# Kernel optimization log

Hardware: AMD Instinct MI355X
Metric: run time of the kernel (lower is better)

## Reference

```python
import jax, jax.numpy as jnp
import numpy as np


def setup_inputs() -> dict:
    key = jax.random.key(0)
    k1, k2, k3, k4 = jax.random.split(key, 4)
    B, S, D, R = 32, 512, 1024, 256
    batch = jax.random.normal(k1, (B, S, D), dtype=jnp.float32)
    # params initialized uniform(-0.05, 0.05) in the original
    proj_L = jax.random.uniform(k2, (D, R), minval=-0.05, maxval=0.05, dtype=jnp.float32)
    proj_R = jax.random.uniform(k3, (R, D), minval=-0.05, maxval=0.05, dtype=jnp.float32)
    bias = jax.random.uniform(k4, (1,), minval=-0.05, maxval=0.05, dtype=jnp.float32)
    return {"batch": batch, "proj_L": proj_L, "proj_R": proj_R, "bias": bias}


def reference(batch, proj_L, proj_R, bias):
    # logits[b,i,j] = batch[b,i] @ (L @ R) @ batch[b,j] + bias
    # Computed as (batch @ L) @ (batch @ R^T)^T -- two batched GEMMs,
    # avoiding the O(B*S^2*D) expanded intermediate of the original.
    # Dropout is identity in eval mode.
    left = jnp.einsum('bsd,dr->bsr', batch, proj_L)   # [B,S,R]
    right = jnp.einsum('rd,btd->brt', proj_R, batch)  # [B,R,S]
    logits = jnp.einsum('bsr,brt->bst', left, right) + bias[0]
    return logits
```

## Files before the change

### kernel.cpp

```cpp
#include <hip/hip_runtime.h>
#include <hip/hip_bf16.h>
#include <stdint.h>

typedef __attribute__((ext_vector_type(8))) __bf16 bf16x8;
typedef __attribute__((ext_vector_type(4))) float f32x4;

static constexpr int Bb = 32, Ss = 512, Dd = 1024, Rr = 256;

__device__ __forceinline__ void gload_lds16(const void* g, void* l) {
  __builtin_amdgcn_global_load_lds(
      (const __attribute__((address_space(1))) void*)g,
      (__attribute__((address_space(3))) void*)l, 16, 0, 0);
}

__global__ __launch_bounds__(256) void prep_kernel(
    const float* __restrict__ L, const float* __restrict__ R,
    __bf16* __restrict__ Bt) {
  int i = blockIdx.x * 256 + threadIdx.x;
  int n = i >> 10;
  int d = i & (Dd - 1);
  float v = (n < Rr) ? L[d * Rr + n] : R[(size_t)(n - Rr) * Dd + d];
  Bt[i] = (__bf16)v;
}

__global__ __launch_bounds__(256, 3) void proj_gemm(
    const float* __restrict__ batch,
    const __bf16* __restrict__ Bt,
    __bf16* __restrict__ outL,
    __bf16* __restrict__ outR) {
  const int s = ((blockIdx.x & 7) << 7) + (blockIdx.x >> 3);
  const int mt = s >> 2;
  const int nt = s & 3;
  const int m0 = mt * 64, n0 = nt * 128;

  __shared__ __align__(16) char smem[49152];

  const int t = threadIdx.x;
  const int lane = t & 63;
  const int wave = t >> 6;
  const int wr = wave >> 1, wc = wave & 1;

  f32x4 acc[2][4] = {};
  f32x4 areg[4];

  const int arow = t >> 2, ag = t & 3;
  const int ags = ag ^ (arow & 7);

  auto issueA = [&](int k0) {
    const float* src = batch + (size_t)(m0 + arow) * Dd + k0 + ag * 8;
    areg[0] = *(const f32x4*)src;
    areg[1] = *(const f32x4*)(src + 4);
    areg[2] = *(const f32x4*)(src + 32);
    areg[3] = *(const f32x4*)(src + 36);
  };
  auto writeA = [&](int buf) {
    char* Ab = smem + buf * 8192;
    bf16x8 v0, v1;
    v0[0] = (__bf16)areg[0][0]; v0[1] = (__bf16)areg[0][1];
    v0[2] = (__bf16)areg[0][2]; v0[3] = (__bf16)areg[0][3];
    v0[4] = (__bf16)areg[1][0]; v0[5] = (__bf16)areg[1][1];
    v0[6] = (__bf16)areg[1][2]; v0[7] = (__bf16)areg[1][3];
    v1[0] = (__bf16)areg[2][0]; v1[1] = (__bf16)areg[2][1];
    v1[2] = (__bf16)areg[2][2]; v1[3] = (__bf16)areg[2][3];
    v1[4] = (__bf16)areg[3][0]; v1[5] = (__bf16)areg[3][1];
    v1[6] = (__bf16)areg[3][2]; v1[7] = (__bf16)areg[3][3];
    *(bf16x8*)(Ab + (arow * 8 + ags) * 16) = v0;
    *(bf16x8*)(Ab + (arow * 8 + (ags ^ 4)) * 16) = v1;
  };
  auto stageB = [&](int buf, int k0) {
    char* Bbuf = smem + 16384 + buf * 16384;
#pragma unroll
    for (int p = 0; p < 4; ++p) {
      int e = p * 256 + t;
      int row = e >> 3, g = e & 7;
      int gs = g ^ (row & 7);
      gload_lds16(Bt + (size_t)(n0 + row) * Dd + k0 + gs * 8,
                  Bbuf + e * 16);
    }
  };
  auto compute = [&](int buf) {
    const char* Ab = smem + buf * 8192;
    const char* Bbuf = smem + 16384 + buf * 16384;
#pragma unroll
    for (int kk = 0; kk < 2; ++kk) {
      const int g = kk * 4 + (lane >> 4);
      bf16x8 a[2], b[4];
#pragma unroll
      for (int m = 0; m < 2; ++m) {
        int row = wr * 32 + m * 16 + (lane & 15);
        a[m] = *(const bf16x8*)(Ab + (row * 8 + (g ^ (row & 7))) * 16);
      }
#pragma unroll
      for (int n = 0; n < 4; ++n) {
        int row = wc * 64 + n * 16 + (lane & 15);
        b[n] = *(const bf16x8*)(Bbuf + (row * 8 + (g ^ (row & 7))) * 16);
      }
#pragma unroll
      for (int m = 0; m < 2; ++m)
#pragma unroll
        for (int n = 0; n < 4; ++n)
          acc[m][n] = __builtin_amdgcn_mfma_f32_16x16x32_bf16(a[m], b[n],
                                                              acc[m][n], 0, 0, 0);
    }
  };

  issueA(0);
  stageB(0, 0);
  writeA(0);
  __syncthreads();

#pragma unroll 1
  for (int tt = 0; tt < 16; ++tt) {
    const int buf = tt & 1;
    if (tt < 15) {
      issueA(tt * 64 + 64);
      stageB(buf ^ 1, tt * 64 + 64);
    }
    compute(buf);
    if (tt < 15) writeA(buf ^ 1);
    __syncthreads();
  }

  __bf16* out = (n0 < Rr) ? outL : outR;
  const int cb = n0 & (Rr - 1);
  const int col = lane & 15, rgrp = lane >> 4;
#pragma unroll
  for (int m = 0; m < 2; ++m) {
    int r0 = m0 + wr * 32 + m * 16 + rgrp * 4;
#pragma unroll
    for (int n = 0; n < 4; ++n) {
      int c = cb + wc * 64 + n * 16 + col;
#pragma unroll
      for (int i = 0; i < 4; ++i)
        out[(size_t)(r0 + i) * Rr + c] = (__bf16)acc[m][n][i];
    }
  }
}

__global__ __launch_bounds__(256, 4) void score_gemm(
    const __bf16* __restrict__ left,
    const __bf16* __restrict__ right,
    const float* __restrict__ biasp,
    float* __restrict__ out) {
  const int nt = blockIdx.x;
  const int mt = blockIdx.y;
  const int bz = blockIdx.z;
  const __bf16* A = left + (size_t)bz * Ss * Rr;
  const __bf16* B = right + (size_t)bz * Ss * Rr;
  float* O = out + (size_t)bz * Ss * Ss;
  const int m0 = mt * 64, n0 = nt * 128;

  __shared__ __align__(16) char smem[24576];

  const int t = threadIdx.x;
  const int lane = t & 63;
  const int wave = t >> 6;
  const int wr = wave >> 1, wc = wave & 1;

  f32x4 acc[2][4] = {};

  for (int it = 0; it < 4; ++it) {
    const int k0 = it * 64;
    __syncthreads();
#pragma unroll
    for (int q = 0; q < 2; ++q) {
      int e = q * 256 + t;
      int row = e >> 3, g = e & 7;
      int gsrc = g ^ (row & 7);
      gload_lds16(A + (size_t)(m0 + row) * Rr + k0 + gsrc * 8, smem + e * 16);
    }
#pragma unroll
    for (int q = 0; q < 4; ++q) {
      int e = q * 256 + t;
      int row = e >> 3, g = e & 7;
      int gsrc = g ^ (row & 7);
      gload_lds16(B + (size_t)(n0 + row) * Rr + k0 + gsrc * 8,
                  smem + 8192 + e * 16);
    }
    __syncthreads();

#pragma unroll
    for (int kk = 0; kk < 2; ++kk) {
      bf16x8 a[2], b[4];
#pragma unroll
      for (int m = 0; m < 2; ++m) {
        int row = wr * 32 + m * 16 + (lane & 15);
        int g = kk * 4 + (lane >> 4);
        a[m] = *(const bf16x8*)(smem + (row * 8 + (g ^ (row & 7))) * 16);
      }
#pragma unroll
      for (int n = 0; n < 4; ++n) {
        int row = wc * 64 + n * 16 + (lane & 15);
        int g = kk * 4 + (lane >> 4);
        b[n] = *(const bf16x8*)(smem + 8192 +
                                (row * 8 + (g ^ (row & 7))) * 16);
      }
#pragma unroll
      for (int m = 0; m < 2; ++m)
#pragma unroll
        for (int n = 0; n < 4; ++n)
          acc[m][n] = __builtin_amdgcn_mfma_f32_16x16x32_bf16(a[m], b[n],
                                                              acc[m][n], 0, 0, 0);
    }
  }

  const float bias = *biasp;
  const int col = lane & 15, rgrp = lane >> 4;
#pragma unroll
  for (int m = 0; m < 2; ++m) {
    int r0 = m0 + wr * 32 + m * 16 + rgrp * 4;
#pragma unroll
    for (int n = 0; n < 4; ++n) {
      int c = n0 + wc * 64 + n * 16 + col;
#pragma unroll
      for (int i = 0; i < 4; ++i)
        O[(size_t)(r0 + i) * Ss + c] = acc[m][n][i] + bias;
    }
  }
}

extern "C" void kernel_launch(void* const* d_in, const int* in_sizes, int n_in,
                              void* d_out, int out_size, void* d_ws,
                              size_t ws_size, hipStream_t stream) {
  const float* batch = (const float*)d_in[0];
  const float* projL = (const float*)d_in[1];
  const float* projR = (const float*)d_in[2];
  const float* bias = (const float*)d_in[3];
  float* out = (float*)d_out;

  char* ws = (char*)d_ws;
  __bf16* left = (__bf16*)(ws);
  __bf16* right = (__bf16*)(ws + 8388608);
  __bf16* Btc = (__bf16*)(ws + 16777216);

  prep_kernel<<<dim3(2048), dim3(256), 0, stream>>>(projL, projR, Btc);
  proj_gemm<<<dim3(1024), dim3(256), 0, stream>>>(batch, Btc, left, right);
  score_gemm<<<dim3(4, 8, 32), dim3(256), 0, stream>>>(left, right, bias, out);
}
```

Before: 54.05 us.

## Pre-convert batch to bf16 and use larger-tile bf16 projection GEMM

Adds a separate kernel that converts the fp32 batch to bf16 in workspace. A new projection GEMM then loads bf16 A and B tiles directly into LDS with global_load_lds, using 128x128 tiles and a 4x4 MFMA accumulator per wave. This removes the register-staged fp32-to-bf16 conversion inside the GEMM and raises arithmetic intensity per tile. The cost is an extra pass that writes and rereads a 32MB bf16 copy, plus a single-buffered K loop with two barriers per step. The old fp32 path is kept as a fallback when the workspace is too small.

```diff
diff --git a/kernel.cpp b/kernel.cpp
--- a/kernel.cpp
+++ b/kernel.cpp
@@ -23,7 +23,91 @@
   Bt[i] = (__bf16)v;
 }
 
-__global__ __launch_bounds__(256, 3) void proj_gemm(
+__global__ __launch_bounds__(256) void conv_kernel(
+    const float* __restrict__ batch, __bf16* __restrict__ batchbf) {
+  size_t base = ((size_t)blockIdx.x * 256 + threadIdx.x) * 8;
+  f32x4 f0 = *(const f32x4*)(batch + base);
+  f32x4 f1 = *(const f32x4*)(batch + base + 4);
+  bf16x8 v;
+  v[0] = (__bf16)f0[0]; v[1] = (__bf16)f0[1];
+  v[2] = (__bf16)f0[2]; v[3] = (__bf16)f0[3];
+  v[4] = (__bf16)f1[0]; v[5] = (__bf16)f1[1];
+  v[6] = (__bf16)f1[2]; v[7] = (__bf16)f1[3];
+  *(bf16x8*)(batchbf + base) = v;
+}
+
+__global__ __launch_bounds__(256, 3) void proj_gemm_bf(
+    const __bf16* __restrict__ Abf,
+    const __bf16* __restrict__ Bt,
+    __bf16* __restrict__ outL,
+    __bf16* __restrict__ outR) {
+  const int s = ((blockIdx.x & 7) << 6) + (blockIdx.x >> 3);
+  const int mt = s >> 2;
+  const int nt = s & 3;
+  const int m0 = mt * 128, n0 = nt * 128;
+
+  __shared__ __align__(16) char smem[16384];
+  char* Ab = smem;
+  char* Bbuf = smem + 8192;
+
+  const int t = threadIdx.x;
+  const int lane = t & 63;
+  const int wave = t >> 6;
+  const int wr = wave >> 1, wc = wave & 1;
+
+  f32x4 acc[4][4] = {};
+
+#pragma unroll 1
+  for (int it = 0; it < 32; ++it) {
+    const int k0 = it * 32;
+    __syncthreads();
+#pragma unroll
+    for (int p = 0; p < 2; ++p) {
+      int e = p * 256 + t;
+      int row = e >> 2, g = e & 3;
+      int gs = g ^ ((row >> 1) & 3);
+      gload_lds16(Abf + (size_t)(m0 + row) * Dd + k0 + gs * 8, Ab + e * 16);
+      gload_lds16(Bt + (size_t)(n0 + row) * Dd + k0 + gs * 8, Bbuf + e * 16);
+    }
+    __syncthreads();
+
+    const int g = lane >> 4;
+    bf16x8 a[4], b[4];
+#pragma unroll
+    for (int m = 0; m < 4; ++m) {
+      int row = wr * 64 + m * 16 + (lane & 15);
+      a[m] = *(const bf16x8*)(Ab + (row * 4 + (g ^ ((row >> 1) & 3))) * 16);
+    }
+#pragma unroll
+    for (int n = 0; n < 4; ++n) {
+      int row = wc * 64 + n * 16 + (lane & 15);
+      b[n] = *(const bf16x8*)(Bbuf + (row * 4 + (g ^ ((row >> 1) & 3))) * 16);
+    }
+#pragma unroll
+    for (int m = 0; m < 4; ++m)
+#pragma unroll
+      for (int n = 0; n < 4; ++n)
+        acc[m][n] = __builtin_amdgcn_mfma_f32_16x16x32_bf16(a[m], b[n],
+                                                            acc[m][n], 0, 0, 0);
+  }
+
+  __bf16* out = (n0 < Rr) ? outL : outR;
+  const int cb = n0 & (Rr - 1);
+  const int col = lane & 15, rgrp = lane >> 4;
+#pragma unroll
+  for (int m = 0; m < 4; ++m) {
+    int r0 = m0 + wr * 64 + m * 16 + rgrp * 4;
+#pragma unroll
+    for (int n = 0; n < 4; ++n) {
+      int c = cb + wc * 64 + n * 16 + col;
+#pragma unroll
+      for (int i = 0; i < 4; ++i)
+        out[(size_t)(r0 + i) * Rr + c] = (__bf16)acc[m][n][i];
+    }
+  }
+}
+
+__global__ __launch_bounds__(256, 3) void proj_gemm_f32(
     const float* __restrict__ batch,
     const __bf16* __restrict__ Bt,
     __bf16* __restrict__ outL,
@@ -34,7 +118,6 @@
   const int m0 = mt * 64, n0 = nt * 128;
 
   __shared__ __align__(16) char smem[49152];
-
   const int t = threadIdx.x;
   const int lane = t & 63;
   const int wave = t >> 6;
@@ -42,7 +125,6 @@
 
   f32x4 acc[2][4] = {};
   f32x4 areg[4];
-
   const int arow = t >> 2, ag = t & 3;
   const int ags = ag ^ (arow & 7);
 
@@ -74,8 +156,7 @@
       int e = p * 256 + t;
       int row = e >> 3, g = e & 7;
       int gs = g ^ (row & 7);
-      gload_lds16(Bt + (size_t)(n0 + row) * Dd + k0 + gs * 8,
-                  Bbuf + e * 16);
+      gload_lds16(Bt + (size_t)(n0 + row) * Dd + k0 + gs * 8, Bbuf + e * 16);
     }
   };
   auto compute = [&](int buf) {
@@ -108,7 +189,6 @@
   stageB(0, 0);
   writeA(0);
   __syncthreads();
-
 #pragma unroll 1
   for (int tt = 0; tt < 16; ++tt) {
     const int buf = tt & 1;
@@ -151,7 +231,6 @@
   const int m0 = mt * 64, n0 = nt * 128;
 
   __shared__ __align__(16) char smem[24576];
-
   const int t = threadIdx.x;
   const int lane = t & 63;
   const int wave = t >> 6;
@@ -232,8 +311,17 @@
   __bf16* left = (__bf16*)(ws);
   __bf16* right = (__bf16*)(ws + 8388608);
   __bf16* Btc = (__bf16*)(ws + 16777216);
+  __bf16* batchbf = (__bf16*)(ws + 17825792);
+  const size_t WS_NEED = 17825792ull + 33554432ull;
 
   prep_kernel<<<dim3(2048), dim3(256), 0, stream>>>(projL, projR, Btc);
-  proj_gemm<<<dim3(1024), dim3(256), 0, stream>>>(batch, Btc, left, right);
+  if (ws_size >= WS_NEED) {
+    conv_kernel<<<dim3(8192), dim3(256), 0, stream>>>(batch, batchbf);
+    proj_gemm_bf<<<dim3(512), dim3(256), 0, stream>>>(batchbf, Btc, left,
+                                                      right);
+  } else {
+    proj_gemm_f32<<<dim3(1024), dim3(256), 0, stream>>>(batch, Btc, left,
+                                                        right);
+  }
   score_gemm<<<dim3(4, 8, 32), dim3(256), 0, stream>>>(left, right, bias, out);
 }
```

Result: slower. 62.06 us (+14.8%).
